# Kernel tuning notes

Measured on AMD Instinct MI355X. Metric: run time of the kernel, lower is better.

The kernel has to match this reference:

```python
import jax, jax.numpy as jnp
import numpy as np

DEFAULT_MASK_VALUE = -0.7 * float(jnp.finfo(jnp.dtype('float32')).max)


def setup_inputs() -> dict:
    key = jax.random.key(0)
    k1, k2, k3, k4 = jax.random.split(key, 4)
    B, T, NQ, NKV, D = 2, 2048, 32, 8, 128
    query = jax.random.normal(k1, (B, T, NQ, D), dtype=jnp.float32)
    k = jax.random.normal(k2, (B, T, NKV, D), dtype=jnp.float32)
    v = jax.random.normal(k3, (B, T, NKV, D), dtype=jnp.float32)
    # packed-sequence segment ids: sorted small ints so segments are contiguous
    decoder_segment_ids = jnp.sort(jax.random.randint(k4, (B, T), 0, 4), axis=-1).astype(jnp.int32)
    return {"query": query, "key": k, "value": v, "decoder_segment_ids": decoder_segment_ids}


def _generate_attention_mask(q_seq_len, kv_seq_len, decoder_segment_ids):
    # segment mask: [b, 1, 1, t, s]
    seg = (decoder_segment_ids[:, :, None] == decoder_segment_ids[:, None, :])[:, None, None, :, :]
    # causal mask: [1, 1, 1, t, s]
    row = jax.lax.broadcasted_iota(jnp.int32, (q_seq_len, kv_seq_len), 0)
    col = jax.lax.broadcasted_iota(jnp.int32, (q_seq_len, kv_seq_len), 1)
    causal = (col <= row)[None, None, None, :, :]
    mask = jnp.logical_and(seg, causal)
    return jnp.where(mask, 0.0, DEFAULT_MASK_VALUE)


def _apply_mask_to_logits(logits, mask):
    return jnp.where(mask >= DEFAULT_MASK_VALUE * 0.5, logits, DEFAULT_MASK_VALUE)


def reference(query, key, value, decoder_segment_ids):
    b, t, n, d = query.shape
    n_kv = key.shape[2]
    g = n // n_kv  # query heads per kv head (GQA)
    q = query.reshape(b, t, n_kv, g, d)
    # qk product (no internal sqrt(d) scaling, matching AttentionOp.qk_product)
    logits = jnp.einsum('btkgd,bskd->bkgts', q, key)  # [b, n_kv, g, t, s]
    mask = _generate_attention_mask(t, key.shape[1], decoder_segment_ids)
    logits = _apply_mask_to_logits(logits, mask)
    weights = jax.nn.softmax(logits, axis=-1).astype(query.dtype)
    out = jnp.einsum('bkgts,bskd->btkgd', weights, value)
    return out.reshape(b, t, n, d)
```

## Files before the change

### kernel.cpp

```cpp
#include <hip/hip_runtime.h>


typedef __bf16 bf16x8 __attribute__((ext_vector_type(8)));
typedef __bf16 bf16x2 __attribute__((ext_vector_type(2)));
typedef _Float16 f16x8 __attribute__((ext_vector_type(8)));
typedef float f32x4 __attribute__((ext_vector_type(4)));
typedef unsigned int uint2v __attribute__((ext_vector_type(2)));

#define B_   2
#define T_   2048
#define NQ_  32
#define NKV_ 8
#define D_   128

#define MASKV (-3.0e38f)
#define LOG2E 1.44269504f
#define TILE_US 8192
#define WS_TILES_BYTES ((size_t)B_ * NKV_ * (T_ / 32) * TILE_US * 2)
#define WS_NEED (WS_TILES_BYTES + (size_t)B_ * T_ * 4)

static __device__ __forceinline__ unsigned short f2bf(float x) {
    union { float f; unsigned int u; } c; c.f = x;
    unsigned int r = c.u + 0x7fffu + ((c.u >> 16) & 1u);
    return (unsigned short)(r >> 16);
}

union U8  { unsigned short us[8]; bf16x8 v; };
union H8  { _Float16 h[8]; f16x8 v; };
union PKW { bf16x2 h; unsigned int u; };
union PA4 { unsigned int u[4]; bf16x8 v; };

static __device__ __forceinline__ void dma16(const unsigned short* g, unsigned short* l) {
    __builtin_amdgcn_global_load_lds(
        (const __attribute__((address_space(1))) unsigned int*)g,
        (__attribute__((address_space(3))) unsigned int*)l, 16, 0, 0);
}

static __device__ __forceinline__ void pl32swap(unsigned int& a, unsigned int& b) {
#if __has_builtin(__builtin_amdgcn_permlane32_swap)
    uint2v t = __builtin_amdgcn_permlane32_swap(a, b, false, false);
    a = t.x; b = t.y;
#else
    asm("s_nop 1\n\tv_permlane32_swap_b32 %0, %1" : "+v"(a), "+v"(b));
#endif
}
static __device__ __forceinline__ void pl16swap(unsigned int& a, unsigned int& b) {
#if __has_builtin(__builtin_amdgcn_permlane16_swap)
    uint2v t = __builtin_amdgcn_permlane16_swap(a, b, false, false);
    a = t.x; b = t.y;
#else
    asm("s_nop 1\n\tv_permlane16_swap_b32 %0, %1" : "+v"(a), "+v"(b));
#endif
}

__global__ __launch_bounds__(256)
void prep(const float* __restrict__ kg, const float* __restrict__ vg,
          unsigned short* __restrict__ ws)
{
    const int tid = threadIdx.x;
    const int st  = blockIdx.x;
    const int kvh = blockIdx.y;
    const int b   = blockIdx.z;
    unsigned short* base = ws + ((size_t)((b * NKV_ + kvh) * (T_ / 32) + st)) * TILE_US;

    #pragma unroll
    for (int it = 0; it < 2; ++it) {
        int task = tid + it * 256;
        int r = task >> 4, c = task & 15;
        const float* kp = kg + (((size_t)(b * T_ + st * 32 + r)) * NKV_ + kvh) * D_ + c * 8;
        H8 hu;
        #pragma unroll
        for (int j = 0; j < 8; ++j) hu.h[j] = (_Float16)kp[j];
        int slot = r * 16 + (c ^ (r & 7));
        *(f16x8*)(base + slot * 8) = hu.v;
    }
    #pragma unroll
    for (int it = 0; it < 2; ++it) {
        int task = tid + it * 256;
        int d = task & 127, sc = task >> 7;
        const float* vp = vg + (((size_t)(b * T_ + st * 32 + sc * 8)) * NKV_ + kvh) * D_ + d;
        U8 pk;
        #pragma unroll
        for (int j = 0; j < 8; ++j) pk.us[j] = f2bf(vp[j * (NKV_ * D_)]);
        int slot = d * 4 + (sc ^ ((d >> 1) & 3));
        *(bf16x8*)(base + 4096 + slot * 8) = pk.v;
    }
}

__global__ __launch_bounds__(256)
void prep_sstart(const int* __restrict__ seg, int* __restrict__ sstart)
{
    int idx = blockIdx.x * 256 + threadIdx.x;
    int b = idx >> 11, t = idx & (T_ - 1);
    const int* sb = seg + b * T_;
    int target = sb[t];
    int lo = 0, hi = t;
    while (lo < hi) { int mid = (lo + hi) >> 1; if (sb[mid] < target) lo = mid + 1; else hi = mid; }
    sstart[idx] = lo;
}

__global__ __launch_bounds__(256)
void attn_fwd(const float* __restrict__ qg,
              const int* __restrict__ sstart,
              const unsigned short* __restrict__ ws,
              float* __restrict__ outg)
{
    __shared__ unsigned short sA[TILE_US];
    __shared__ unsigned short sB[TILE_US];

    const int tid  = threadIdx.x;
    const int wave = tid >> 6;
    const int lane = tid & 63;
    const int qd   = lane >> 4;
    const int ln   = lane & 15;

    const int i    = blockIdx.x;
    const int head = blockIdx.y;
    const int kvh  = head >> 2;
    const int b    = blockIdx.z;

    const unsigned short* wsbase =
        ws + ((size_t)((b * NKV_ + kvh) * (T_ / 32))) * TILE_US;

    int koff[4];
    #pragma unroll
    for (int c = 0; c < 4; ++c)
        koff[c] = (ln * 16 + ((4 * c + qd) ^ (ln & 7))) * 8;
    const int vbase = (ln * 4 + (qd ^ ((ln >> 1) & 3))) * 8;

#define STAGE(dst, tl) do {                                                    \
        const unsigned short* _tb = wsbase + (size_t)(tl) * TILE_US;           \
        _Pragma("unroll")                                                      \
        for (int _i = 0; _i < 4; ++_i)                                         \
            dma16(_tb + ((wave * 4 + _i) * 64 + lane) * 8,                     \
                  (dst) + (wave * 4 + _i) * 512);                              \
    } while (0)

#define COMPUTE(BUF, TL) do {                                                  \
        const unsigned short* _Kf = (BUF);                                     \
        const unsigned short* _Vt = (BUF) + 4096;                              \
        const int _s0 = (TL) * 32;                                             \
        f32x4 S0 = {0.f,0.f,0.f,0.f}, S1 = {0.f,0.f,0.f,0.f};                  \
        __builtin_amdgcn_s_setprio(1);                                         \
        _Pragma("unroll")                                                      \
        for (int c = 0; c < 4; ++c) {                                          \
            f16x8 k0 = *(const f16x8*)(_Kf + koff[c]);                         \
            f16x8 k1 = *(const f16x8*)(_Kf + koff[c] + 2048);                  \
            S0 = __builtin_amdgcn_mfma_f32_16x16x32_f16(k0, qh[c], S0,0,0,0);  \
            S1 = __builtin_amdgcn_mfma_f32_16x16x32_f16(k1, qh[c], S1,0,0,0);  \
            S0 = __builtin_amdgcn_mfma_f32_16x16x32_f16(k0, ql[c], S0,0,0,0);  \
            S1 = __builtin_amdgcn_mfma_f32_16x16x32_f16(k1, ql[c], S1,0,0,0);  \
        }                                                                      \
        __builtin_amdgcn_s_setprio(0);                                         \
        bf16x8 bv[8];                                                          \
        _Pragma("unroll")                                                      \
        for (int sub = 0; sub < 8; ++sub)                                      \
            bv[sub] = *(const bf16x8*)(_Vt + vbase + sub * 512);               \
        float p0[4], p1[4];                                                    \
        if (_s0 >= wave_rs_max && _s0 + 31 <= wave_row_min) {                  \
            _Pragma("unroll")                                                  \
            for (int r = 0; r < 4; ++r) {                                      \
                p0[r] = exp2f(S0[r]);                                          \
                p1[r] = exp2f(S1[r]);                                          \
            }                                                                  \
        } else {                                                               \
            _Pragma("unroll")                                                  \
            for (int r = 0; r < 4; ++r) {                                      \
                int kv0 = _s0 + qd * 4 + r;                                    \
                int kv1 = kv0 + 16;                                            \
                float sv0 = (kv0 >= rs_l && kv0 <= trow_l) ? S0[r] : MASKV;    \
                float sv1 = (kv1 >= rs_l && kv1 <= trow_l) ? S1[r] : MASKV;    \
                p0[r] = exp2f(sv0);                                            \
                p1[r] = exp2f(sv1);                                            \
            }                                                                  \
        }                                                                      \
        l_lane += (p0[0] + p0[1]) + (p0[2] + p0[3])                            \
                + (p1[0] + p1[1]) + (p1[2] + p1[3]);                           \
        PKW c0, c1, c2, c3;                                                    \
        c0.h = (bf16x2){(__bf16)p0[0], (__bf16)p0[1]};                         \
        c1.h = (bf16x2){(__bf16)p0[2], (__bf16)p0[3]};                         \
        c2.h = (bf16x2){(__bf16)p1[0], (__bf16)p1[1]};                         \
        c3.h = (bf16x2){(__bf16)p1[2], (__bf16)p1[3]};                         \
        unsigned int w0 = c0.u, w1 = c1.u, w2 = c2.u, w3 = c3.u;               \
        pl32swap(w0, w2); pl32swap(w1, w3);                                    \
        pl16swap(w0, w2); pl16swap(w1, w3);                                    \
        PA4 pw; pw.u[0] = w0; pw.u[1] = w1; pw.u[2] = w2; pw.u[3] = w3;        \
        bf16x8 pa = pw.v;                                                      \
        __builtin_amdgcn_s_setprio(1);                                         \
        _Pragma("unroll")                                                      \
        for (int sub = 0; sub < 8; ++sub)                                      \
            O[sub] = __builtin_amdgcn_mfma_f32_16x16x32_bf16(pa, bv[sub], O[sub],0,0,0); \
        __builtin_amdgcn_s_setprio(0);                                         \
    } while (0)

    for (int phase = 0; phase < 2; ++phase) {
        const int t0 = (phase == 0 ? (2 * (int)gridDim.x - 1 - i) : i) * 64;

        f16x8 qh[4], ql[4];
        {
            const float* qrow =
                qg + (((size_t)(b * T_ + (t0 + wave * 16 + ln)) * NQ_) + head) * D_;
            #pragma unroll
            for (int c = 0; c < 4; ++c) {
                float4 a  = *(const float4*)(qrow + c * 32 + qd * 8);
                float4 b2 = *(const float4*)(qrow + c * 32 + qd * 8 + 4);
                float xs[8] = {a.x, a.y, a.z, a.w, b2.x, b2.y, b2.z, b2.w};
                H8 hu, lu;
                #pragma unroll
                for (int j = 0; j < 8; ++j) {
                    float x = xs[j] * LOG2E;
                    _Float16 h = (_Float16)x;
                    hu.h[j] = h;
                    lu.h[j] = (_Float16)(x - (float)h);
                }
                qh[c] = hu.v; ql[c] = lu.v;
            }
        }

        const int trow_l = t0 + wave * 16 + ln;
        const int rs_l   = sstart[b * T_ + trow_l];
        int wave_rs_max = rs_l;
        wave_rs_max = max(wave_rs_max, __shfl_xor(wave_rs_max, 1));
        wave_rs_max = max(wave_rs_max, __shfl_xor(wave_rs_max, 2));
        wave_rs_max = max(wave_rs_max, __shfl_xor(wave_rs_max, 4));
        wave_rs_max = max(wave_rs_max, __shfl_xor(wave_rs_max, 8));
        const int wave_row_min = t0 + wave * 16;

        const int tile0   = sstart[b * T_ + t0] >> 5;
        const int n_tiles = t0 / 32 + 2;

        f32x4 O[8];
        #pragma unroll
        for (int k = 0; k < 8; ++k) O[k] = (f32x4){0.f, 0.f, 0.f, 0.f};
        float l_lane = 0.f;

        __syncthreads();

        int t = tile0;
        STAGE(sA, t);
        __syncthreads();
        while (t + 1 < n_tiles) {
            STAGE(sB, t + 1);
            COMPUTE(sA, t);
            __syncthreads();
            if (t + 2 < n_tiles) STAGE(sA, t + 2);
            COMPUTE(sB, t + 1);
            __syncthreads();
            t += 2;
        }
        if (t < n_tiles) COMPUTE(sA, t);

        float l = l_lane;
        l += __shfl_xor(l, 16);
        l += __shfl_xor(l, 32);
        const float invl = 1.0f / l;
        int trow[4];
        float inv[4];
        #pragma unroll
        for (int r = 0; r < 4; ++r) {
            trow[r] = t0 + wave * 16 + qd * 4 + r;
            inv[r]  = __shfl(invl, qd * 4 + r);
        }
        #pragma unroll
        for (int sub = 0; sub < 8; ++sub) {
            #pragma unroll
            for (int r = 0; r < 4; ++r) {
                outg[(((size_t)(b * T_ + trow[r]) * NQ_) + head) * D_ + sub * 16 + ln] =
                    O[sub][r] * inv[r];
            }
        }
    }

#undef STAGE
#undef COMPUTE
}

#define KSTR 136
#define VSTR 40
#define PSTR 40
static __device__ __forceinline__ float bf2f(unsigned short h) {
    union { unsigned int u; float f; } c; c.u = (unsigned int)h << 16; return c.f;
}
__global__ __launch_bounds__(256)
void attn_fwd_fb(const float* __restrict__ qg,
                 const float* __restrict__ kg,
                 const float* __restrict__ vg,
                 const int* __restrict__ seg,
                 float* __restrict__ outg)
{
    __shared__ unsigned short sKh[32 * KSTR];
    __shared__ unsigned short sKl[32 * KSTR];
    __shared__ unsigned short sVt[128 * VSTR];
    __shared__ unsigned short sP[4][16 * PSTR];

    const int tid  = threadIdx.x;
    const int wave = tid >> 6;
    const int lane = tid & 63;
    const int qd   = lane >> 4;
    const int ln   = lane & 15;
    const int t0   = ((int)gridDim.x - 1 - (int)blockIdx.x) * 64;
    const int head = blockIdx.y;
    const int kvh  = head >> 2;
    const int b    = blockIdx.z;

    bf16x8 qh[4], ql[4];
    {
        const float* qrow =
            qg + (((size_t)(b * T_ + (t0 + wave * 16 + ln)) * NQ_) + head) * D_;
        #pragma unroll
        for (int c = 0; c < 4; ++c) {
            float4 a  = *(const float4*)(qrow + c * 32 + qd * 8);
            float4 b2 = *(const float4*)(qrow + c * 32 + qd * 8 + 4);
            float xs[8] = {a.x, a.y, a.z, a.w, b2.x, b2.y, b2.z, b2.w};
            U8 hu, lu;
            #pragma unroll
            for (int j = 0; j < 8; ++j) {
                unsigned short h = f2bf(xs[j]);
                hu.us[j] = h;
                lu.us[j] = f2bf(xs[j] - bf2f(h));
            }
            qh[c] = hu.v; ql[c] = lu.v;
        }
    }
    const int* sb = seg + (size_t)b * T_;
    int qseg[4];
    #pragma unroll
    for (int r = 0; r < 4; ++r) qseg[r] = sb[t0 + wave * 16 + qd * 4 + r];
    int tile0;
    {
        int target = sb[t0];
        int lo = 0, hi = t0;
        while (lo < hi) { int mid = (lo + hi) >> 1; if (sb[mid] < target) lo = mid + 1; else hi = mid; }
        tile0 = lo >> 5;
    }
    f32x4 O[8];
    #pragma unroll
    for (int i = 0; i < 8; ++i) O[i] = (f32x4){0.f, 0.f, 0.f, 0.f};
    float m_prev[4], l_lane[4];
    #pragma unroll
    for (int r = 0; r < 4; ++r) { m_prev[r] = MASKV; l_lane[r] = 0.f; }
    const int n_tiles = t0 / 32 + 2;

    for (int tile = tile0; tile < n_tiles; ++tile) {
        const int s0 = tile * 32;
        __syncthreads();
        #pragma unroll
        for (int it = 0; it < 2; ++it) {
            int task = tid + it * 256;
            int r = task >> 4, d = (task & 15) * 8;
            const float* kp = kg + (((size_t)(b * T_ + s0 + r) * NKV_) + kvh) * D_ + d;
            float4 a  = *(const float4*)(kp);
            float4 b2 = *(const float4*)(kp + 4);
            float xs[8] = {a.x, a.y, a.z, a.w, b2.x, b2.y, b2.z, b2.w};
            U8 hu, lu;
            #pragma unroll
            for (int j = 0; j < 8; ++j) {
                unsigned short h = f2bf(xs[j]);
                hu.us[j] = h;
                lu.us[j] = f2bf(xs[j] - bf2f(h));
            }
            *(bf16x8*)(sKh + r * KSTR + d) = hu.v;
            *(bf16x8*)(sKl + r * KSTR + d) = lu.v;
        }
        #pragma unroll
        for (int it = 0; it < 2; ++it) {
            int task = tid + it * 256;
            int d = task & 127, sg = task >> 7;
            const float* vp = vg + (((size_t)(b * T_ + s0 + sg * 8) * NKV_) + kvh) * D_ + d;
            U8 pk;
            #pragma unroll
            for (int j = 0; j < 8; ++j) pk.us[j] = f2bf(vp[j * (NKV_ * D_)]);
            *(bf16x8*)(sVt + d * VSTR + sg * 8) = pk.v;
        }
        __syncthreads();

        f32x4 S0 = {0.f,0.f,0.f,0.f}, S1 = {0.f,0.f,0.f,0.f};
        #pragma unroll
        for (int c = 0; c < 4; ++c) {
            bf16x8 kh0 = *(const bf16x8*)(sKh + ln * KSTR + c * 32 + qd * 8);
            bf16x8 kh1 = *(const bf16x8*)(sKh + (16 + ln) * KSTR + c * 32 + qd * 8);
            bf16x8 kl0 = *(const bf16x8*)(sKl + ln * KSTR + c * 32 + qd * 8);
            bf16x8 kl1 = *(const bf16x8*)(sKl + (16 + ln) * KSTR + c * 32 + qd * 8);
            S0 = __builtin_amdgcn_mfma_f32_16x16x32_bf16(qh[c], kh0, S0, 0, 0, 0);
            S1 = __builtin_amdgcn_mfma_f32_16x16x32_bf16(qh[c], kh1, S1, 0, 0, 0);
            S0 = __builtin_amdgcn_mfma_f32_16x16x32_bf16(qh[c], kl0, S0, 0, 0, 0);
            S1 = __builtin_amdgcn_mfma_f32_16x16x32_bf16(qh[c], kl1, S1, 0, 0, 0);
            S0 = __builtin_amdgcn_mfma_f32_16x16x32_bf16(ql[c], kh0, S0, 0, 0, 0);
            S1 = __builtin_amdgcn_mfma_f32_16x16x32_bf16(ql[c], kh1, S1, 0, 0, 0);
        }
        const int ks0 = sb[s0 + ln];
        const int ks1 = sb[s0 + 16 + ln];
        float p0[4], p1[4], alpha[4];
        #pragma unroll
        for (int r = 0; r < 4; ++r) {
            const int trow = t0 + wave * 16 + qd * 4 + r;
            float s0v = ((s0 + ln <= trow) && (ks0 == qseg[r])) ? S0[r] : MASKV;
            float s1v = ((s0 + 16 + ln <= trow) && (ks1 == qseg[r])) ? S1[r] : MASKV;
            float mx = fmaxf(s0v, s1v);
            mx = fmaxf(mx, __shfl_xor(mx, 1));
            mx = fmaxf(mx, __shfl_xor(mx, 2));
            mx = fmaxf(mx, __shfl_xor(mx, 4));
            mx = fmaxf(mx, __shfl_xor(mx, 8));
            const float mn = fmaxf(m_prev[r], mx);
            alpha[r] = __expf(m_prev[r] - mn);
            p0[r] = __expf(s0v - mn);
            p1[r] = __expf(s1v - mn);
            l_lane[r] = alpha[r] * l_lane[r] + p0[r] + p1[r];
            m_prev[r] = mn;
        }
        #pragma unroll
        for (int i = 0; i < 8; ++i) {
            O[i][0] *= alpha[0]; O[i][1] *= alpha[1];
            O[i][2] *= alpha[2]; O[i][3] *= alpha[3];
        }
        {
            unsigned short* pw = sP[wave] + (qd * 4) * PSTR + ln;
            #pragma unroll
            for (int r = 0; r < 4; ++r) {
                pw[r * PSTR]      = f2bf(p0[r]);
                pw[r * PSTR + 16] = f2bf(p1[r]);
            }
        }
        asm volatile("s_waitcnt lgkmcnt(0)" ::: "memory");
        bf16x8 pa = *(const bf16x8*)(sP[wave] + ln * PSTR + qd * 8);
        #pragma unroll
        for (int sub = 0; sub < 8; ++sub) {
            bf16x8 bv = *(const bf16x8*)(sVt + (sub * 16 + ln) * VSTR + qd * 8);
            O[sub] = __builtin_amdgcn_mfma_f32_16x16x32_bf16(pa, bv, O[sub], 0, 0, 0);
        }
    }
    float inv[4];
    #pragma unroll
    for (int r = 0; r < 4; ++r) {
        float l = l_lane[r];
        l += __shfl_xor(l, 1);
        l += __shfl_xor(l, 2);
        l += __shfl_xor(l, 4);
        l += __shfl_xor(l, 8);
        inv[r] = 1.0f / l;
    }
    #pragma unroll
    for (int sub = 0; sub < 8; ++sub) {
        #pragma unroll
        for (int r = 0; r < 4; ++r) {
            const int trow = t0 + wave * 16 + qd * 4 + r;
            outg[(((size_t)(b * T_ + trow) * NQ_) + head) * D_ + sub * 16 + ln] =
                O[sub][r] * inv[r];
        }
    }
}

extern "C" void kernel_launch(void* const* d_in, const int* in_sizes, int n_in,
                              void* d_out, int out_size, void* d_ws, size_t ws_size,
                              hipStream_t stream) {
    const float* q  = (const float*)d_in[0];
    const float* k  = (const float*)d_in[1];
    const float* v  = (const float*)d_in[2];
    const int*   sg = (const int*)d_in[3];
    float*       o  = (float*)d_out;
    if (ws_size >= WS_NEED) {
        unsigned short* ws = (unsigned short*)d_ws;
        int* sstart = (int*)((char*)d_ws + WS_TILES_BYTES);
        prep<<<dim3(T_ / 32, NKV_, B_), dim3(256), 0, stream>>>(k, v, ws);
        prep_sstart<<<dim3(B_ * T_ / 256), dim3(256), 0, stream>>>(sg, sstart);
        attn_fwd<<<dim3(T_ / 128, NQ_, B_), dim3(256), 0, stream>>>(q, sstart, ws, o);
    } else {
        attn_fwd_fb<<<dim3(T_ / 64, NQ_, B_), dim3(256), 0, stream>>>(q, k, v, sg, o);
    }
}
```

Measured before the change: 211.0 us.

## Load K/V fragments directly from global into registers, bypassing LDS staging

After: 224.3 us. 1.06x slower.

```diff
diff --git a/kernel.cpp b/kernel.cpp
--- a/kernel.cpp
+++ b/kernel.cpp
@@ -29,12 +29,6 @@
 union H8  { _Float16 h[8]; f16x8 v; };
 union PKW { bf16x2 h; unsigned int u; };
 union PA4 { unsigned int u[4]; bf16x8 v; };
-
-static __device__ __forceinline__ void dma16(const unsigned short* g, unsigned short* l) {
-    __builtin_amdgcn_global_load_lds(
-        (const __attribute__((address_space(1))) unsigned int*)g,
-        (__attribute__((address_space(3))) unsigned int*)l, 16, 0, 0);
-}
 
 static __device__ __forceinline__ void pl32swap(unsigned int& a, unsigned int& b) {
 #if __has_builtin(__builtin_amdgcn_permlane32_swap)
@@ -66,12 +60,13 @@
     #pragma unroll
     for (int it = 0; it < 2; ++it) {
         int task = tid + it * 256;
-        int r = task >> 4, c = task & 15;
-        const float* kp = kg + (((size_t)(b * T_ + st * 32 + r)) * NKV_ + kvh) * D_ + c * 8;
+        int r = task >> 4, c16 = task & 15;
+        const float* kp = kg + (((size_t)(b * T_ + st * 32 + r)) * NKV_ + kvh) * D_ + c16 * 8;
         H8 hu;
         #pragma unroll
         for (int j = 0; j < 8; ++j) hu.h[j] = (_Float16)kp[j];
-        int slot = r * 16 + (c ^ (r & 7));
+        int c = c16 >> 2, qd = c16 & 3, hi = r >> 4, ln = r & 15;
+        int slot = (c * 2 + hi) * 64 + qd * 16 + ln;
         *(f16x8*)(base + slot * 8) = hu.v;
     }
     #pragma unroll
@@ -82,7 +77,7 @@
         U8 pk;
         #pragma unroll
         for (int j = 0; j < 8; ++j) pk.us[j] = f2bf(vp[j * (NKV_ * D_)]);
-        int slot = d * 4 + (sc ^ ((d >> 1) & 3));
+        int slot = (d >> 4) * 64 + sc * 16 + (d & 15);
         *(bf16x8*)(base + 4096 + slot * 8) = pk.v;
     }
 }
@@ -105,9 +100,6 @@
               const unsigned short* __restrict__ ws,
               float* __restrict__ outg)
 {
-    __shared__ unsigned short sA[TILE_US];
-    __shared__ unsigned short sB[TILE_US];
-
     const int tid  = threadIdx.x;
     const int wave = tid >> 6;
     const int lane = tid & 63;
@@ -120,42 +112,32 @@
     const int b    = blockIdx.z;
 
     const unsigned short* wsbase =
-        ws + ((size_t)((b * NKV_ + kvh) * (T_ / 32))) * TILE_US;
-
-    int koff[4];
-    #pragma unroll
-    for (int c = 0; c < 4; ++c)
-        koff[c] = (ln * 16 + ((4 * c + qd) ^ (ln & 7))) * 8;
-    const int vbase = (ln * 4 + (qd ^ ((ln >> 1) & 3))) * 8;
-
-#define STAGE(dst, tl) do {                                                    \
+        ws + ((size_t)((b * NKV_ + kvh) * (T_ / 32))) * TILE_US + lane * 8;
+
+#define LOADKV(KB, VB, tl) do {                                                \
         const unsigned short* _tb = wsbase + (size_t)(tl) * TILE_US;           \
         _Pragma("unroll")                                                      \
-        for (int _i = 0; _i < 4; ++_i)                                         \
-            dma16(_tb + ((wave * 4 + _i) * 64 + lane) * 8,                     \
-                  (dst) + (wave * 4 + _i) * 512);                              \
+        for (int _c = 0; _c < 4; ++_c) {                                       \
+            KB[_c][0] = *(const f16x8*)(_tb + (_c * 2 + 0) * 512);             \
+            KB[_c][1] = *(const f16x8*)(_tb + (_c * 2 + 1) * 512);             \
+        }                                                                      \
+        _Pragma("unroll")                                                      \
+        for (int _s = 0; _s < 8; ++_s)                                         \
+            VB[_s] = *(const bf16x8*)(_tb + 4096 + _s * 512);                  \
     } while (0)
 
-#define COMPUTE(BUF, TL) do {                                                  \
-        const unsigned short* _Kf = (BUF);                                     \
-        const unsigned short* _Vt = (BUF) + 4096;                              \
+#define COMPUTE(KB, VB, TL) do {                                               \
         const int _s0 = (TL) * 32;                                             \
         f32x4 S0 = {0.f,0.f,0.f,0.f}, S1 = {0.f,0.f,0.f,0.f};                  \
         __builtin_amdgcn_s_setprio(1);                                         \
         _Pragma("unroll")                                                      \
         for (int c = 0; c < 4; ++c) {                                          \
-            f16x8 k0 = *(const f16x8*)(_Kf + koff[c]);                         \
-            f16x8 k1 = *(const f16x8*)(_Kf + koff[c] + 2048);                  \
-            S0 = __builtin_amdgcn_mfma_f32_16x16x32_f16(k0, qh[c], S0,0,0,0);  \
-            S1 = __builtin_amdgcn_mfma_f32_16x16x32_f16(k1, qh[c], S1,0,0,0);  \
-            S0 = __builtin_amdgcn_mfma_f32_16x16x32_f16(k0, ql[c], S0,0,0,0);  \
-            S1 = __builtin_amdgcn_mfma_f32_16x16x32_f16(k1, ql[c], S1,0,0,0);  \
+            S0 = __builtin_amdgcn_mfma_f32_16x16x32_f16(KB[c][0], qh[c], S0,0,0,0); \
+            S1 = __builtin_amdgcn_mfma_f32_16x16x32_f16(KB[c][1], qh[c], S1,0,0,0); \
+            S0 = __builtin_amdgcn_mfma_f32_16x16x32_f16(KB[c][0], ql[c], S0,0,0,0); \
+            S1 = __builtin_amdgcn_mfma_f32_16x16x32_f16(KB[c][1], ql[c], S1,0,0,0); \
         }                                                                      \
         __builtin_amdgcn_s_setprio(0);                                         \
-        bf16x8 bv[8];                                                          \
-        _Pragma("unroll")                                                      \
-        for (int sub = 0; sub < 8; ++sub)                                      \
-            bv[sub] = *(const bf16x8*)(_Vt + vbase + sub * 512);               \
         float p0[4], p1[4];                                                    \
         if (_s0 >= wave_rs_max && _s0 + 31 <= wave_row_min) {                  \
             _Pragma("unroll")                                                  \
@@ -189,7 +171,7 @@
         __builtin_amdgcn_s_setprio(1);                                         \
         _Pragma("unroll")                                                      \
         for (int sub = 0; sub < 8; ++sub)                                      \
-            O[sub] = __builtin_amdgcn_mfma_f32_16x16x32_bf16(pa, bv[sub], O[sub],0,0,0); \
+            O[sub] = __builtin_amdgcn_mfma_f32_16x16x32_bf16(pa, VB[sub], O[sub],0,0,0); \
         __builtin_amdgcn_s_setprio(0);                                         \
     } while (0)
 
@@ -234,21 +216,19 @@
         for (int k = 0; k < 8; ++k) O[k] = (f32x4){0.f, 0.f, 0.f, 0.f};
         float l_lane = 0.f;
 
-        __syncthreads();
+        f16x8  kA[4][2], kB_[4][2];
+        bf16x8 vA[8], vB_[8];
 
         int t = tile0;
-        STAGE(sA, t);
-        __syncthreads();
+        LOADKV(kA, vA, t);
         while (t + 1 < n_tiles) {
-            STAGE(sB, t + 1);
-            COMPUTE(sA, t);
-            __syncthreads();
-            if (t + 2 < n_tiles) STAGE(sA, t + 2);
-            COMPUTE(sB, t + 1);
-            __syncthreads();
+            LOADKV(kB_, vB_, t + 1);
+            COMPUTE(kA, vA, t);
+            if (t + 2 < n_tiles) LOADKV(kA, vA, t + 2);
+            COMPUTE(kB_, vB_, t + 1);
             t += 2;
         }
-        if (t < n_tiles) COMPUTE(sA, t);
+        if (t < n_tiles) COMPUTE(kA, vA, t);
 
         float l = l_lane;
         l += __shfl_xor(l, 16);
@@ -271,7 +251,7 @@
         }
     }
 
-#undef STAGE
+#undef LOADKV
 #undef COMPUTE
 }
 
```
